# Performance work log

Hardware: AMD Instinct MI355X
Metric: run time of the kernel (lower is better)

Reference implementation:

```python
import jax, jax.numpy as jnp
import numpy as np

H, HS, C = 16, 64, 1024  # num_heads, head_size, n_embd

def setup_inputs() -> dict:
    key = jax.random.key(0)
    ks = jax.random.split(key, 5)
    B, T = 2, 2048
    s = 1.0 / np.sqrt(C)
    return {
        "x": jax.random.normal(ks[0], (B, T, C), dtype=jnp.float32),
        "Wq": jax.random.normal(ks[1], (H, C, HS), dtype=jnp.float32) * s,
        "Wk": jax.random.normal(ks[2], (H, C, HS), dtype=jnp.float32) * s,
        "Wv": jax.random.normal(ks[3], (H, C, HS), dtype=jnp.float32) * s,
        "Wo": jax.random.normal(ks[4], (C, C), dtype=jnp.float32) * s,
    }

def reference(x, Wq, Wk, Wv, Wo):
    B, T, Cdim = x.shape
    scale = Cdim ** -0.5  # original scales by n_embd**-0.5, not head_size
    q = jnp.einsum('btc,hcd->bhtd', x, Wq)
    k = jnp.einsum('btc,hcd->bhtd', x, Wk)
    v = jnp.einsum('btc,hcd->bhtd', x, Wv)
    wei = jnp.einsum('bhtd,bhsd->bhts', q, k) * scale  # [B,H,T,T]
    causal = jnp.tril(jnp.ones((T, T), dtype=bool))
    wei = jnp.where(causal, wei, -jnp.inf)
    wei = jax.nn.softmax(wei, axis=-1)
    out = jnp.einsum('bhts,bhsd->bhtd', wei, v)  # [B,H,T,HS]
    out = out.transpose(0, 2, 1, 3).reshape(B, T, -1)  # concat heads -> [B,T,C]
    return out @ Wo.T
```

## Files before the change

kernel.cpp:

```cpp
#include <hip/hip_runtime.h>

typedef unsigned short ushort_t;
typedef __bf16 bf16x8 __attribute__((ext_vector_type(8)));
typedef float f32x4 __attribute__((ext_vector_type(4)));
typedef float f32x16 __attribute__((ext_vector_type(16)));
typedef unsigned short ushortx8 __attribute__((ext_vector_type(8)));
typedef unsigned int uintx4 __attribute__((ext_vector_type(4)));

#define NH 16
#define HS 64
#define CD 1024
#define NB 2
#define NT 2048
#define BT (NB * NT)
#define N3 (3 * CD)

#define L2E_DIV32 0.04508422002778011f

#define QKV_LD 2048
#define SLOT_BYTES 18432
#define WAVE_BYTES 4608
#define R0_SLOTS 796

__constant__ static const int QB_TAB[51] = {
  0,1,2, 3,3, 4,4, 5,5, 6,6,6, 7,7,7, 8,8,8,
  9,9,9,9, 10,10,10,10, 11,11,11,11,
  12,12,12,12,12, 13,13,13,13,13, 14,14,14,14,14,
  15,15,15,15,15,15};
__constant__ static const int K_TAB[51] = {
  1,1,1, 2,2, 2,2, 2,2, 3,3,3, 3,3,3, 3,3,3,
  4,4,4,4, 4,4,4,4, 4,4,4,4,
  5,5,5,5,5, 5,5,5,5,5, 5,5,5,5,5,
  6,6,6,6,6,6};
__constant__ static const int T0_TAB[51] = {
  0, 0, 0, 0,4, 0,5, 0,6, 0,5,10, 0,6,11, 0,6,12,
  0,5,10,15, 0,6,12,17, 0,6,12,18,
  0,6,11,16,21, 0,6,12,18,23, 0,6,12,18,24,
  0,6,12,17,22,27};
__constant__ static const int T1_TAB[51] = {
  2, 4, 6, 4,8, 5,10, 6,12, 5,10,14, 6,11,16, 6,12,18,
  5,10,15,20, 6,12,17,22, 6,12,18,24,
  6,11,16,21,26, 6,12,18,23,28, 6,12,18,24,30,
  6,12,17,22,27,32};
__constant__ static const int FIRSTC_TAB[16] = {
  0,1,2,3,5,7,9,12,15,18,22,26,30,35,40,45};


__device__ __forceinline__ ushort_t bf16_rne(float f) {
  union { float f; unsigned u; } v; v.f = f;
  unsigned u = v.u;
  unsigned r = (u + 0x7FFFu + ((u >> 16) & 1u)) >> 16;
  return (ushort_t)r;
}

__device__ __forceinline__ float bf2f(ushort_t u) {
  union { unsigned u; float f; } v; v.u = ((unsigned)u) << 16; return v.f;
}

__device__ __forceinline__ void gload_lds16(const ushort_t* g, ushort_t* l) {
  __builtin_amdgcn_global_load_lds(
      (const __attribute__((address_space(1))) unsigned int*)g,
      (__attribute__((address_space(3))) unsigned int*)l, 16, 0, 0);
}

__device__ __forceinline__ f32x4 mfma16(ushortx8 a, ushortx8 b, f32x4 c) {
  return __builtin_amdgcn_mfma_f32_16x16x32_bf16(
      __builtin_bit_cast(bf16x8, a), __builtin_bit_cast(bf16x8, b), c, 0, 0, 0);
}

__device__ __forceinline__ f32x16 mfma32(ushortx8 a, ushortx8 b, f32x16 c) {
  return __builtin_amdgcn_mfma_f32_32x32x16_bf16(
      __builtin_bit_cast(bf16x8, a), __builtin_bit_cast(bf16x8, b), c, 0, 0, 0);
}

__device__ __forceinline__ unsigned cvt_pk_bf16(float lo, float hi) {
  unsigned r;
  asm("v_cvt_pk_bf16_f32 %0, %1, %2" : "=v"(r) : "v"(lo), "v"(hi));
  return r;
}

__device__ __forceinline__ void plswap(unsigned &a, unsigned &b) {
  asm volatile("v_permlane32_swap_b32 %0, %1" : "+v"(a), "+v"(b));
}

__device__ __forceinline__ const char* slot_ptr(const char* wsb, const char* dout, int s) {
  return (s < R0_SLOTS) ? wsb + (size_t)s * SLOT_BYTES
                        : dout + (size_t)(s - R0_SLOTS) * SLOT_BYTES;
}


__global__ __launch_bounds__(256)
void pack_cast(const float4* __restrict__ in, ushort_t* __restrict__ out, int n4) {
  const int i = blockIdx.x * 256 + threadIdx.x;
  if (i >= n4) return;
  const float4 v = in[i];
  ushort4 r;
  r.x = bf16_rne(v.x); r.y = bf16_rne(v.y);
  r.z = bf16_rne(v.z); r.w = bf16_rne(v.w);
  *(ushort4*)(out + (size_t)i * 4) = r;
}

__global__ __launch_bounds__(256)
void pack_wqkv(const float* __restrict__ Wq, const float* __restrict__ Wk,
               const float* __restrict__ Wv, ushort_t* __restrict__ out) {
  __shared__ ushort_t tile[64 * 66];
  const int sh = blockIdx.y;
  const int s = sh >> 4, h = sh & 15;
  const float* W = (s == 0) ? Wq : ((s == 1) ? Wk : Wv);
  const int c0 = blockIdx.x * 64;
  const int t = threadIdx.x;
#pragma unroll
  for (int j = 0; j < 16; ++j) {
    const int idx = t + j * 256;
    const int ci = idx >> 6, d = idx & 63;
    const float v = W[(size_t)(h * 1024 + c0 + ci) * 64 + d];
    tile[d * 66 + ci] = bf16_rne(v);
  }
  __syncthreads();
#pragma unroll
  for (int j = 0; j < 16; ++j) {
    const int idx = t + j * 256;
    const int d = idx >> 6, ci = idx & 63;
    out[(size_t)(s * 1024 + h * 64 + d) * 1024 + c0 + ci] = tile[d * 66 + ci];
  }
}


template <int MODE>
__global__ __launch_bounds__(256)
void gemm_bt(const ushort_t* __restrict__ A, const ushort_t* __restrict__ Bt,
             void* __restrict__ Cv, ushort_t* __restrict__ Vt,
             int M, int N, int K) {
  __shared__ __align__(16) ushort_t ldsA[2][128 * 32];
  __shared__ __align__(16) ushort_t ldsB[2][128 * 32];
  const int tid = threadIdx.x;
  const int lane = tid & 63;
  const int wave = tid >> 6;
  const int row0 = blockIdx.y * 128;
  const int col0 = blockIdx.x * 128;
  const int wm = wave >> 1, wn = wave & 1;

  f32x4 acc[4][4] = {};

  const int ce = (tid & 3) * 8;

  auto stage = [&](int buf, int kt) {
    const int kbase = kt * 32;
#pragma unroll
    for (int j = 0; j < 2; ++j) {
      const int r = j * 64 + (tid >> 2);
      gload_lds16(A + (size_t)(row0 + r) * K + kbase + ce,
                  &ldsA[buf][(j * 256 + wave * 64) * 8]);
      gload_lds16(Bt + (size_t)(col0 + r) * K + kbase + ce,
                  &ldsB[buf][(j * 256 + wave * 64) * 8]);
    }
  };

  const int arow_off = (wm * 64 + (lane & 15)) * 32 + (lane >> 4) * 8;
  const int brow_off = (wn * 64 + (lane & 15)) * 32 + (lane >> 4) * 8;

  auto compute = [&](int buf) {
    ushortx8 af[4], bfr[4];
#pragma unroll
    for (int m = 0; m < 4; ++m)
      af[m] = *(const ushortx8*)&ldsA[buf][arow_off + m * 512];
#pragma unroll
    for (int n = 0; n < 4; ++n)
      bfr[n] = *(const ushortx8*)&ldsB[buf][brow_off + n * 512];
#pragma unroll
    for (int m = 0; m < 4; ++m)
#pragma unroll
      for (int n = 0; n < 4; ++n)
        acc[m][n] = mfma16(af[m], bfr[n], acc[m][n]);
  };

  stage(0, 0);
  __syncthreads();
  const int nk = K >> 5;
  for (int kt = 0; kt < nk; ++kt) {
    const int cur = kt & 1;
    if (kt + 1 < nk) stage(cur ^ 1, kt + 1);
    compute(cur);
    __syncthreads();
  }

#pragma unroll
  for (int m = 0; m < 4; ++m) {
    const int rbase = row0 + wm * 64 + m * 16 + (lane >> 4) * 4;
#pragma unroll
    for (int n = 0; n < 4; ++n) {
      const int col = col0 + wn * 64 + n * 16 + (lane & 15);
      if constexpr (MODE == 0) {
#pragma unroll
        for (int i = 0; i < 4; ++i)
          ((float*)Cv)[(size_t)(rbase + i) * N + col] = acc[m][n][i];
      } else {
        if (col < 2048) {
          const float sc = (col < 1024) ? L2E_DIV32 : 1.0f;
#pragma unroll
          for (int i = 0; i < 4; ++i)
            ((ushort_t*)Cv)[(size_t)(rbase + i) * QKV_LD + col] =
                bf16_rne(acc[m][n][i] * sc);
        } else {
          const int dcol = col - 2048;
          const int bI = rbase >> 11;
          const int t0i = rbase & 2047;
          ushort4 pk;
          pk.x = bf16_rne(acc[m][n][0]);
          pk.y = bf16_rne(acc[m][n][1]);
          pk.z = bf16_rne(acc[m][n][2]);
          pk.w = bf16_rne(acc[m][n][3]);
          *(ushort4*)(Vt + (size_t)(bI * 1024 + dcol) * NT + t0i) = pk;
        }
      }
    }
  }
}


__global__ __launch_bounds__(256, 3)
void attn_fwd8(const ushort_t* __restrict__ QKV, const ushort_t* __restrict__ Vt,
               ushort_t* __restrict__ O, char* __restrict__ wsb,
               char* __restrict__ dout) {
  __shared__ __align__(16) ushort_t KV[3][2][4096];

  const int tid = threadIdx.x;
  const int lane = tid & 63;
  const int w = tid >> 6;
  const int l31 = lane & 31;
  const int h = lane >> 5;

  const int x = blockIdx.x;
  const int bh = x & 31;
  const int c = 50 - (x >> 5);
  const int qb = QB_TAB[c];
  const int k  = K_TAB[c];
  const int t0 = T0_TAB[c];
  const int t1 = T1_TAB[c];
  const int nt = 2 * qb + 2;
  const bool lastc = (t1 == nt);

  const int b = bh >> 4, head = bh & 15;
  const size_t base = (size_t)b * NT * QKV_LD;
  const int qg = qb * 128 + w * 32 + l31;
  const int tmax = lastc ? (2 * qb + (w >> 1)) : (t1 - 1);

  ushortx8 qf[4];
  {
    const ushort_t* qp = QKV + base + (size_t)qg * QKV_LD + head * 64 + h * 8;
#pragma unroll
    for (int kc = 0; kc < 4; ++kc) qf[kc] = *(const ushortx8*)(qp + kc * 16);
  }
  asm volatile("s_waitcnt vmcnt(0)" ::: "memory");

  int koff[4];
#pragma unroll
  for (int kc = 0; kc < 4; ++kc)
    koff[kc] = l31 * 128 + (((2 * kc + h) ^ (l31 & 7)) * 16);

  const int rowA = tid >> 3, ccA = tid & 7;
  const int rowB = 32 + rowA;
  const ushort_t* kg = QKV + base + 1024 + head * 64;
  const ushort_t* vg = Vt + (size_t)(bh * 64) * NT;
  const ushort_t* ksA = kg + (size_t)(t0 * 64 + rowA) * QKV_LD + ((ccA ^ (rowA & 7)) * 8);
  const ushort_t* ksB = kg + (size_t)(t0 * 64 + rowB) * QKV_LD + ((ccA ^ (rowB & 7)) * 8);
  const ushort_t* vsA = vg + (size_t)rowA * NT + t0 * 64 + ((ccA ^ (rowA & 7)) * 8);
  const ushort_t* vsB = vg + (size_t)rowB * NT + t0 * 64 + ((ccA ^ (rowB & 7)) * 8);
  const size_t kadv = (size_t)64 * QKV_LD;

  f32x16 oA = {}, oB = {};
  float m_r = -INFINITY, l_r = 0.f;

  gload_lds16(ksA, &KV[0][0][w * 512]);
  gload_lds16(ksB, &KV[0][0][2048 + w * 512]);
  gload_lds16(vsA, &KV[0][1][w * 512]);
  gload_lds16(vsB, &KV[0][1][2048 + w * 512]);

  int cur = 0;
  for (int t = t0; t < t1; ++t) {
    int nxt = cur + 1; if (nxt == 3) nxt = 0;
    if (t + 1 < t1) {
      ksA += kadv; ksB += kadv; vsA += 64; vsB += 64;
      gload_lds16(ksA, &KV[nxt][0][w * 512]);
      gload_lds16(ksB, &KV[nxt][0][2048 + w * 512]);
      gload_lds16(vsA, &KV[nxt][1][w * 512]);
      gload_lds16(vsB, &KV[nxt][1][2048 + w * 512]);
      asm volatile("s_waitcnt vmcnt(4)" ::: "memory");
    } else {
      asm volatile("s_waitcnt vmcnt(0)" ::: "memory");
    }
    __builtin_amdgcn_s_barrier();
    asm volatile("" ::: "memory");

    if (t <= tmax) {
      const bool diag = lastc && (t == tmax);
      const bool halfB = diag && ((w & 1) == 0);
      const char* kb = (const char*)&KV[cur][0][0];
      const char* vb = (const char*)&KV[cur][1][0];

      f32x16 sA = {}, sB = {};
#pragma unroll
      for (int kc = 0; kc < 4; ++kc)
        sA = mfma32(*(const ushortx8*)(kb + koff[kc]), qf[kc], sA);
      if (!halfB) {
#pragma unroll
        for (int kc = 0; kc < 4; ++kc)
          sB = mfma32(*(const ushortx8*)(kb + 4096 + koff[kc]), qf[kc], sB);
      }

      if (diag) {
#pragma unroll
        for (int r = 0; r < 16; ++r) {
          const int krow = (r & 3) + 8 * (r >> 2) + 4 * h;
          if (halfB) { if (krow > l31) sA[r] = -INFINITY; }
          else       { if (krow > l31) sB[r] = -INFINITY; }
        }
      }

      float mm[16];
#pragma unroll
      for (int r = 0; r < 16; ++r) mm[r] = halfB ? sA[r] : fmaxf(sA[r], sB[r]);
#pragma unroll
      for (int st = 8; st >= 1; st >>= 1)
#pragma unroll
        for (int r = 0; r < st; ++r) mm[r] = fmaxf(mm[r], mm[r + st]);
      const float mx = fmaxf(mm[0], __shfl_xor(mm[0], 32, 64));

      if (__any(mx > m_r + 8.0f)) {
        const float mn = fmaxf(m_r, mx);
        const float al = exp2f(m_r - mn);
        m_r = mn; l_r *= al;
#pragma unroll
        for (int r = 0; r < 16; ++r) { oA[r] *= al; oB[r] *= al; }
      }

      unsigned u[16];
      float ps[8];
#pragma unroll
      for (int jj = 0; jj < 8; ++jj) {
        const float e0 = exp2f(sA[2 * jj] - m_r);
        const float e1 = exp2f(sA[2 * jj + 1] - m_r);
        u[jj] = cvt_pk_bf16(e0, e1);
        ps[jj] = e0 + e1;
      }
      if (!halfB) {
#pragma unroll
        for (int jj = 0; jj < 8; ++jj) {
          const float e0 = exp2f(sB[2 * jj] - m_r);
          const float e1 = exp2f(sB[2 * jj + 1] - m_r);
          u[8 + jj] = cvt_pk_bf16(e0, e1);
          ps[jj] += e0 + e1;
        }
      }
#pragma unroll
      for (int st = 4; st >= 1; st >>= 1)
#pragma unroll
        for (int r = 0; r < st; ++r) ps[r] += ps[r + st];
      l_r += ps[0] + __shfl_xor(ps[0], 32, 64);

      plswap(u[0], u[2]);   plswap(u[1], u[3]);
      plswap(u[4], u[6]);   plswap(u[5], u[7]);
      if (!halfB) {
        plswap(u[8], u[10]);  plswap(u[9], u[11]);
        plswap(u[12], u[14]); plswap(u[13], u[15]);
      }

#pragma unroll
      for (int kc = 0; kc < 4; ++kc) {
        if (kc < 2 || !halfB) {
          uintx4 pw;
          pw[0] = u[4 * kc + 0]; pw[1] = u[4 * kc + 1];
          pw[2] = u[4 * kc + 2]; pw[3] = u[4 * kc + 3];
          const ushortx8 pav = __builtin_bit_cast(ushortx8, pw);
          oA = mfma32(*(const ushortx8*)(vb + koff[kc]), pav, oA);
          oB = mfma32(*(const ushortx8*)(vb + 4096 + koff[kc]), pav, oB);
        }
      }
    }

    cur = nxt;
  }

  if (k == 1) {
    const float inv_l = 1.0f / l_r;
    ushort_t* op = O + ((size_t)(b * NT + qg)) * 1024 + head * 64;
#pragma unroll
    for (int db = 0; db < 2; ++db)
#pragma unroll
      for (int g = 0; g < 4; ++g) {
        ushort4 pk;
        pk.x = bf16_rne((db ? oB[4 * g + 0] : oA[4 * g + 0]) * inv_l);
        pk.y = bf16_rne((db ? oB[4 * g + 1] : oA[4 * g + 1]) * inv_l);
        pk.z = bf16_rne((db ? oB[4 * g + 2] : oA[4 * g + 2]) * inv_l);
        pk.w = bf16_rne((db ? oB[4 * g + 3] : oA[4 * g + 3]) * inv_l);
        *(ushort4*)(op + db * 32 + 8 * g + 4 * h) = pk;
      }
  } else {
    const int s = bh * 51 + c;
    char* wb = (char*)slot_ptr(wsb, dout, s) + w * WAVE_BYTES;
#pragma unroll
    for (int g = 0; g < 4; ++g) {
      ushortx8 pk;
#pragma unroll
      for (int e2 = 0; e2 < 8; ++e2)
        pk[e2] = bf16_rne(g < 2 ? oA[g * 8 + e2] : oB[(g - 2) * 8 + e2]);
      *(ushortx8*)(wb + lane * 64 + g * 16) = pk;
    }
    *(float*)(wb + 4096 + lane * 4) = m_r;
    *(float*)(wb + 4352 + lane * 4) = l_r;
  }
}

__global__ __launch_bounds__(256)
void attn_merge(const char* __restrict__ wsb, const char* __restrict__ dout,
                ushort_t* __restrict__ O) {
  const int x = blockIdx.x;
  const int bh = x & 31;
  const int qb = 3 + (x >> 5);
  const int f = FIRSTC_TAB[qb];
  const int k = K_TAB[f];
  const int tid = threadIdx.x;
  const int lane = tid & 63;
  const int w = tid >> 6;
  const int l31 = lane & 31;
  const int h = lane >> 5;
  const int sbase = bh * 51 + f;

  float M = -INFINITY;
  for (int jj = 0; jj < k; ++jj) {
    const char* wb = slot_ptr(wsb, dout, sbase + jj) + w * WAVE_BYTES;
    M = fmaxf(M, *(const float*)(wb + 4096 + lane * 4));
  }
  float o[32];
#pragma unroll
  for (int r = 0; r < 32; ++r) o[r] = 0.f;
  float lacc = 0.f;
  for (int jj = 0; jj < k; ++jj) {
    const char* wb = slot_ptr(wsb, dout, sbase + jj) + w * WAVE_BYTES;
    const float a = exp2f(*(const float*)(wb + 4096 + lane * 4) - M);
    lacc += a * *(const float*)(wb + 4352 + lane * 4);
#pragma unroll
    for (int g = 0; g < 4; ++g) {
      const ushortx8 v = *(const ushortx8*)(wb + lane * 64 + g * 16);
#pragma unroll
      for (int e = 0; e < 8; ++e) o[g * 8 + e] += a * bf2f(v[e]);
    }
  }
  const float inv_l = 1.0f / lacc;
  const int b = bh >> 4, head = bh & 15;
  const int qg = qb * 128 + w * 32 + l31;
  ushort_t* op = O + ((size_t)(b * NT + qg)) * 1024 + head * 64;
#pragma unroll
  for (int db = 0; db < 2; ++db)
#pragma unroll
    for (int g = 0; g < 4; ++g) {
      ushort4 pk;
      pk.x = bf16_rne(o[db * 16 + 4 * g + 0] * inv_l);
      pk.y = bf16_rne(o[db * 16 + 4 * g + 1] * inv_l);
      pk.z = bf16_rne(o[db * 16 + 4 * g + 2] * inv_l);
      pk.w = bf16_rne(o[db * 16 + 4 * g + 3] * inv_l);
      *(ushort4*)(op + db * 32 + 8 * g + 4 * h) = pk;
    }
}


extern "C" void kernel_launch(void* const* d_in, const int* in_sizes, int n_in,
                              void* d_out, int out_size, void* d_ws, size_t ws_size,
                              hipStream_t stream) {
  (void)in_sizes; (void)n_in; (void)out_size; (void)ws_size;
  const float* x  = (const float*)d_in[0];
  const float* Wq = (const float*)d_in[1];
  const float* Wk = (const float*)d_in[2];
  const float* Wv = (const float*)d_in[3];
  const float* Wo = (const float*)d_in[4];

  char* ws = (char*)d_ws;
  ushort_t* Xbf    = (ushort_t*)(ws);
  ushort_t* Wqkv_t = (ushort_t*)(ws + 8388608);
  ushort_t* Wo_bf  = (ushort_t*)(ws + 14680064);
  ushort_t* QKV    = (ushort_t*)(ws + 16777216);
  ushort_t* Vt     = (ushort_t*)(ws + 33554432);
  ushort_t* Obf    = (ushort_t*)(ws + 41943040);

  pack_cast<<<4096, 256, 0, stream>>>((const float4*)x, Xbf, 1048576);
  pack_cast<<<1024, 256, 0, stream>>>((const float4*)Wo, Wo_bf, 262144);
  pack_wqkv<<<dim3(16, 48), 256, 0, stream>>>(Wq, Wk, Wv, Wqkv_t);

  gemm_bt<1><<<dim3(24, 32), 256, 0, stream>>>(Xbf, Wqkv_t, QKV, Vt, BT, N3, CD);
  attn_fwd8<<<1632, 256, 0, stream>>>(QKV, Vt, Obf, ws, (char*)d_out);
  attn_merge<<<416, 256, 0, stream>>>(ws, (char*)d_out, Obf);
  gemm_bt<0><<<dim3(8, 32), 256, 0, stream>>>(Obf, Wo_bf, d_out, nullptr, BT, CD, CD);
}
```

Measured before the change: 133.5 us.

## Split attention tile into two 32-key halves with double-buffered LDS

The attention kernel now processes each 64-key tile as two 32-key halves, each doing its own QK MFMA, online-softmax update and PV MFMA. The live score registers drop from two f32x16 to one. LDS buffering goes from triple to double buffering, with an extra barrier at the end of each iteration, so launch bounds can be raised to 4 blocks per CU. The Q fragment load is also moved after the first K/V prefetch so the two overlap. In exchange there are twice as many max/rescale checks and a second barrier per tile, and the shallower prefetch pipeline is less able to hide global-memory latency.

```diff
diff --git a/kernel.cpp b/kernel.cpp
--- a/kernel.cpp
+++ b/kernel.cpp
@@ -218,11 +218,11 @@
 }
 
 
-__global__ __launch_bounds__(256, 3)
-void attn_fwd8(const ushort_t* __restrict__ QKV, const ushort_t* __restrict__ Vt,
+__global__ __launch_bounds__(256, 4)
+void attn_fwd9(const ushort_t* __restrict__ QKV, const ushort_t* __restrict__ Vt,
                ushort_t* __restrict__ O, char* __restrict__ wsb,
                char* __restrict__ dout) {
-  __shared__ __align__(16) ushort_t KV[3][2][4096];
+  __shared__ __align__(16) ushort_t KV[2][2][4096];
 
   const int tid = threadIdx.x;
   const int lane = tid & 63;
@@ -245,14 +245,6 @@
   const int qg = qb * 128 + w * 32 + l31;
   const int tmax = lastc ? (2 * qb + (w >> 1)) : (t1 - 1);
 
-  ushortx8 qf[4];
-  {
-    const ushort_t* qp = QKV + base + (size_t)qg * QKV_LD + head * 64 + h * 8;
-#pragma unroll
-    for (int kc = 0; kc < 4; ++kc) qf[kc] = *(const ushortx8*)(qp + kc * 16);
-  }
-  asm volatile("s_waitcnt vmcnt(0)" ::: "memory");
-
   int koff[4];
 #pragma unroll
   for (int kc = 0; kc < 4; ++kc)
@@ -268,17 +260,73 @@
   const ushort_t* vsB = vg + (size_t)rowB * NT + t0 * 64 + ((ccA ^ (rowB & 7)) * 8);
   const size_t kadv = (size_t)64 * QKV_LD;
 
-  f32x16 oA = {}, oB = {};
-  float m_r = -INFINITY, l_r = 0.f;
-
   gload_lds16(ksA, &KV[0][0][w * 512]);
   gload_lds16(ksB, &KV[0][0][2048 + w * 512]);
   gload_lds16(vsA, &KV[0][1][w * 512]);
   gload_lds16(vsB, &KV[0][1][2048 + w * 512]);
 
-  int cur = 0;
+  ushortx8 qf[4];
+  {
+    const ushort_t* qp = QKV + base + (size_t)qg * QKV_LD + head * 64 + h * 8;
+#pragma unroll
+    for (int kc = 0; kc < 4; ++kc) qf[kc] = *(const ushortx8*)(qp + kc * 16);
+  }
+
+  f32x16 oA = {}, oB = {};
+  float m_r = -INFINITY, l_r = 0.f;
+
+  auto half_pass = [&](f32x16 s, const char* vb, const int kc0, const bool msk) {
+    if (msk) {
+#pragma unroll
+      for (int r = 0; r < 16; ++r) {
+        const int krow = (r & 3) + 8 * (r >> 2) + 4 * h;
+        if (krow > l31) s[r] = -INFINITY;
+      }
+    }
+    float mm[8];
+#pragma unroll
+    for (int r = 0; r < 8; ++r) mm[r] = fmaxf(s[r], s[r + 8]);
+#pragma unroll
+    for (int st = 4; st >= 1; st >>= 1)
+#pragma unroll
+      for (int r = 0; r < st; ++r) mm[r] = fmaxf(mm[r], mm[r + st]);
+    const float mx = fmaxf(mm[0], __shfl_xor(mm[0], 32, 64));
+    if (__any(mx > m_r + 8.0f)) {
+      const float mn = fmaxf(m_r, mx);
+      const float al = exp2f(m_r - mn);
+      m_r = mn; l_r *= al;
+#pragma unroll
+      for (int r = 0; r < 16; ++r) { oA[r] *= al; oB[r] *= al; }
+    }
+    unsigned u[8];
+    float ps[4];
+#pragma unroll
+    for (int jj = 0; jj < 4; ++jj) ps[jj] = 0.f;
+#pragma unroll
+    for (int jj = 0; jj < 8; ++jj) {
+      const float e0 = exp2f(s[2 * jj] - m_r);
+      const float e1 = exp2f(s[2 * jj + 1] - m_r);
+      u[jj] = cvt_pk_bf16(e0, e1);
+      ps[jj & 3] += e0 + e1;
+    }
+    ps[0] += ps[2]; ps[1] += ps[3]; ps[0] += ps[1];
+    l_r += ps[0] + __shfl_xor(ps[0], 32, 64);
+    plswap(u[0], u[2]); plswap(u[1], u[3]);
+    plswap(u[4], u[6]); plswap(u[5], u[7]);
+#pragma unroll
+    for (int q2 = 0; q2 < 2; ++q2) {
+      uintx4 pw;
+      pw[0] = u[4 * q2 + 0]; pw[1] = u[4 * q2 + 1];
+      pw[2] = u[4 * q2 + 2]; pw[3] = u[4 * q2 + 3];
+      const ushortx8 pav = __builtin_bit_cast(ushortx8, pw);
+      oA = mfma32(*(const ushortx8*)(vb + koff[kc0 + q2]), pav, oA);
+      oB = mfma32(*(const ushortx8*)(vb + 4096 + koff[kc0 + q2]), pav, oB);
+    }
+  };
+
+  int curb = 0;
   for (int t = t0; t < t1; ++t) {
-    int nxt = cur + 1; if (nxt == 3) nxt = 0;
+    const int nxt = curb ^ 1;
     if (t + 1 < t1) {
       ksA += kadv; ksB += kadv; vsA += 64; vsB += 64;
       gload_lds16(ksA, &KV[nxt][0][w * 512]);
@@ -295,90 +343,28 @@
     if (t <= tmax) {
       const bool diag = lastc && (t == tmax);
       const bool halfB = diag && ((w & 1) == 0);
-      const char* kb = (const char*)&KV[cur][0][0];
-      const char* vb = (const char*)&KV[cur][1][0];
-
-      f32x16 sA = {}, sB = {};
-#pragma unroll
-      for (int kc = 0; kc < 4; ++kc)
-        sA = mfma32(*(const ushortx8*)(kb + koff[kc]), qf[kc], sA);
+      const char* kb = (const char*)&KV[curb][0][0];
+      const char* vb = (const char*)&KV[curb][1][0];
+
+      {
+        f32x16 sA = {};
+#pragma unroll
+        for (int kc = 0; kc < 4; ++kc)
+          sA = mfma32(*(const ushortx8*)(kb + koff[kc]), qf[kc], sA);
+        half_pass(sA, vb, 0, diag && halfB);
+      }
       if (!halfB) {
+        f32x16 sB = {};
 #pragma unroll
         for (int kc = 0; kc < 4; ++kc)
           sB = mfma32(*(const ushortx8*)(kb + 4096 + koff[kc]), qf[kc], sB);
+        half_pass(sB, vb, 2, diag);
       }
-
-      if (diag) {
-#pragma unroll
-        for (int r = 0; r < 16; ++r) {
-          const int krow = (r & 3) + 8 * (r >> 2) + 4 * h;
-          if (halfB) { if (krow > l31) sA[r] = -INFINITY; }
-          else       { if (krow > l31) sB[r] = -INFINITY; }
-        }
-      }
-
-      float mm[16];
-#pragma unroll
-      for (int r = 0; r < 16; ++r) mm[r] = halfB ? sA[r] : fmaxf(sA[r], sB[r]);
-#pragma unroll
-      for (int st = 8; st >= 1; st >>= 1)
-#pragma unroll
-        for (int r = 0; r < st; ++r) mm[r] = fmaxf(mm[r], mm[r + st]);
-      const float mx = fmaxf(mm[0], __shfl_xor(mm[0], 32, 64));
-
-      if (__any(mx > m_r + 8.0f)) {
-        const float mn = fmaxf(m_r, mx);
-        const float al = exp2f(m_r - mn);
-        m_r = mn; l_r *= al;
-#pragma unroll
-        for (int r = 0; r < 16; ++r) { oA[r] *= al; oB[r] *= al; }
-      }
-
-      unsigned u[16];
-      float ps[8];
-#pragma unroll
-      for (int jj = 0; jj < 8; ++jj) {
-        const float e0 = exp2f(sA[2 * jj] - m_r);
-        const float e1 = exp2f(sA[2 * jj + 1] - m_r);
-        u[jj] = cvt_pk_bf16(e0, e1);
-        ps[jj] = e0 + e1;
-      }
-      if (!halfB) {
-#pragma unroll
-        for (int jj = 0; jj < 8; ++jj) {
-          const float e0 = exp2f(sB[2 * jj] - m_r);
-          const float e1 = exp2f(sB[2 * jj + 1] - m_r);
-          u[8 + jj] = cvt_pk_bf16(e0, e1);
-          ps[jj] += e0 + e1;
-        }
-      }
-#pragma unroll
-      for (int st = 4; st >= 1; st >>= 1)
-#pragma unroll
-        for (int r = 0; r < st; ++r) ps[r] += ps[r + st];
-      l_r += ps[0] + __shfl_xor(ps[0], 32, 64);
-
-      plswap(u[0], u[2]);   plswap(u[1], u[3]);
-      plswap(u[4], u[6]);   plswap(u[5], u[7]);
-      if (!halfB) {
-        plswap(u[8], u[10]);  plswap(u[9], u[11]);
-        plswap(u[12], u[14]); plswap(u[13], u[15]);
-      }
-
-#pragma unroll
-      for (int kc = 0; kc < 4; ++kc) {
-        if (kc < 2 || !halfB) {
-          uintx4 pw;
-          pw[0] = u[4 * kc + 0]; pw[1] = u[4 * kc + 1];
-          pw[2] = u[4 * kc + 2]; pw[3] = u[4 * kc + 3];
-          const ushortx8 pav = __builtin_bit_cast(ushortx8, pw);
-          oA = mfma32(*(const ushortx8*)(vb + koff[kc]), pav, oA);
-          oB = mfma32(*(const ushortx8*)(vb + 4096 + koff[kc]), pav, oB);
-        }
-      }
-    }
-
-    cur = nxt;
+    }
+
+    __builtin_amdgcn_s_barrier();
+    asm volatile("" ::: "memory");
+    curb ^= 1;
   }
 
   if (k == 1) {
@@ -487,7 +473,7 @@
   pack_wqkv<<<dim3(16, 48), 256, 0, stream>>>(Wq, Wk, Wv, Wqkv_t);
 
   gemm_bt<1><<<dim3(24, 32), 256, 0, stream>>>(Xbf, Wqkv_t, QKV, Vt, BT, N3, CD);
-  attn_fwd8<<<1632, 256, 0, stream>>>(QKV, Vt, Obf, ws, (char*)d_out);
+  attn_fwd9<<<1632, 256, 0, stream>>>(QKV, Vt, Obf, ws, (char*)d_out);
   attn_merge<<<416, 256, 0, stream>>>(ws, (char*)d_out, Obf);
   gemm_bt<0><<<dim3(8, 32), 256, 0, stream>>>(Obf, Wo_bf, d_out, nullptr, BT, CD, CD);
 }
```

Result: no change. 131.0 us (-1.8%).
